# Optimization experiments

Measured on AMD Instinct MI355X. Metric: run time of the kernel, lower is better.

## Reference

```python
import jax, jax.numpy as jnp
import numpy as np

D_MODEL = 2048
N_HEADS = 32
N_KV_HEADS = 8
HEAD_DIM = D_MODEL // N_HEADS  # 64
N_REP = N_HEADS // N_KV_HEADS  # 4
SCALE = HEAD_DIM ** -0.5


def _rope_tables(seq_len):
    inv_freq = 1.0 / (10000.0 ** (jnp.arange(0, HEAD_DIM, 2, dtype=jnp.float32) / HEAD_DIM))
    t = jnp.arange(seq_len, dtype=jnp.float32)
    freqs = jnp.outer(t, inv_freq)  # [S, HEAD_DIM/2]
    return jnp.cos(freqs), jnp.sin(freqs)


def _apply_rope(x, cos, sin):
    # x: [b, h, s, d]; interleaved even/odd rotation, matching torch stack+flatten
    x_r, x_i = x[..., ::2], x[..., 1::2]
    out_r = x_r * cos - x_i * sin
    out_i = x_r * sin + x_i * cos
    out = jnp.stack([out_r, out_i], axis=-1)  # [b,h,s,d/2,2]
    return out.reshape(x.shape)


def setup_inputs() -> dict:
    key = jax.random.key(0)
    ks = jax.random.split(key, 5)
    bs, seq_len = 2, 2048
    std = D_MODEL ** -0.5
    x = jax.random.normal(ks[0], (bs, seq_len, D_MODEL), dtype=jnp.float32)
    wq = jax.random.normal(ks[1], (N_HEADS * HEAD_DIM, D_MODEL), dtype=jnp.float32) * std
    wk = jax.random.normal(ks[2], (N_KV_HEADS * HEAD_DIM, D_MODEL), dtype=jnp.float32) * std
    wv = jax.random.normal(ks[3], (N_KV_HEADS * HEAD_DIM, D_MODEL), dtype=jnp.float32) * std
    wo = jax.random.normal(ks[4], (D_MODEL, N_HEADS * HEAD_DIM), dtype=jnp.float32) * std
    return {"x": x, "wq": wq, "wk": wk, "wv": wv, "wo": wo}


def reference(x, wq, wk, wv, wo):
    bs, seq_len, _ = x.shape
    # fused-style QKV projections (nn.Linear: x @ W.T)
    q = (x @ wq.T).reshape(bs, seq_len, N_HEADS, HEAD_DIM).transpose(0, 2, 1, 3)
    k = (x @ wk.T).reshape(bs, seq_len, N_KV_HEADS, HEAD_DIM).transpose(0, 2, 1, 3)
    v = (x @ wv.T).reshape(bs, seq_len, N_KV_HEADS, HEAD_DIM).transpose(0, 2, 1, 3)
    cos, sin = _rope_tables(seq_len)  # [S, HEAD_DIM/2], broadcast over b,h
    q = _apply_rope(q, cos, sin)
    k = _apply_rope(k, cos, sin)
    # GQA: repeat KV heads to match Q heads
    k = jnp.repeat(k, N_REP, axis=1)  # [b, H, s, d]
    v = jnp.repeat(v, N_REP, axis=1)
    attn = jnp.einsum('bhqd,bhkd->bhqk', q, k) * SCALE
    causal = jnp.triu(jnp.ones((seq_len, seq_len), dtype=bool), k=1)
    attn = jnp.where(causal, -jnp.inf, attn)
    attn = jax.nn.softmax(attn, axis=-1)
    out = jnp.einsum('bhqk,bhkd->bhqd', attn, v)
    out = out.transpose(0, 2, 1, 3).reshape(bs, seq_len, D_MODEL)
    return out @ wo.T
```

## Files before the change

kernel.cpp:

```cpp
#include <hip/hip_runtime.h>

#define SEQ    2048
#define DM     2048
#define QKVN   3072
#define VTR    64

typedef short s16x8 __attribute__((ext_vector_type(8)));
typedef float f32x4 __attribute__((ext_vector_type(4)));
typedef unsigned short us;

#define MFMA(a,b,c) __builtin_amdgcn_mfma_f32_16x16x32_bf16((a),(b),(c),0,0,0)

__device__ __forceinline__ float bf2f(us u) {
    unsigned v = ((unsigned)u) << 16;
    return __builtin_bit_cast(float, v);
}
__device__ __forceinline__ us f2bf(float f) {
    unsigned u = __builtin_bit_cast(unsigned, f);
    u += 0x7FFFu + ((u >> 16) & 1u);
    return (us)(u >> 16);
}
__device__ __forceinline__ void stp(us* p, float f) {
    *p = (us)(__builtin_bit_cast(unsigned, f) >> 16);
}
__device__ __forceinline__ void glds16(const us* g, us* l) {
    __builtin_amdgcn_global_load_lds((__attribute__((address_space(1))) void*)g,
                                     (__attribute__((address_space(3))) void*)l, 16, 0, 0);
}

__global__ __launch_bounds__(256) void cvt_all(const float* __restrict__ x,
                                               const float* __restrict__ wq,
                                               const float* __restrict__ wk,
                                               const float* __restrict__ wv,
                                               const float* __restrict__ wo,
                                               us* __restrict__ xb,
                                               us* __restrict__ wdst) {
    int i = (blockIdx.x * blockDim.x + threadIdx.x) * 2;
    const float* src;
    int off;
    if (i < 2097152)      { src = x;  off = 0; }
    else {
        int j = i - 2097152;
        if (j < 1048576)      { src = wq; off = 2097152; }
        else if (j < 1310720) { src = wk; off = 2097152 + 1048576; }
        else if (j < 1572864) { src = wv; off = 2097152 + 1310720; }
        else                  { src = wo; off = 2097152 + 1572864; }
    }
    const int base = i - off;
    float4 v0 = ((const float4*)src)[base];
    float4 v1 = ((const float4*)src)[base + 1];
    s16x8 o;
    o[0] = (short)f2bf(v0.x); o[1] = (short)f2bf(v0.y);
    o[2] = (short)f2bf(v0.z); o[3] = (short)f2bf(v0.w);
    o[4] = (short)f2bf(v1.x); o[5] = (short)f2bf(v1.y);
    o[6] = (short)f2bf(v1.z); o[7] = (short)f2bf(v1.w);
    us* d = (i < 2097152) ? xb : wdst;
    const int di = (i < 2097152) ? i : i - 2097152;
    *(s16x8*)(d + di * 4) = o;
}

template <typename OutT, bool ROPE>
__global__ __launch_bounds__(512) void gemm_bt2(const us* __restrict__ A, const us* __restrict__ W,
                                                OutT* __restrict__ C, us* __restrict__ vt,
                                                int M, int N, int K) {
    __shared__ us lA[2][2][128 * 64];
    __shared__ us lB[2][2][128 * 64];
    const int tid = threadIdx.x, lane = tid & 63, wave = tid >> 6;
    const int quad = lane >> 4, lr = lane & 15;
    const int mh = wave >> 2;
    const int wnx = wave & 3;
    const int bh = wnx >> 1, br0 = (wnx & 1) * 64;
    const int m0 = blockIdx.x * 256, n0 = blockIdx.y * 256;

    const int srow = tid >> 3;
    const int scol = ((tid & 7) ^ (srow & 7)) * 8;
    const int sdst = srow * 64 + (tid & 7) * 8;

    const us* gA = A + (size_t)m0 * K;
    const us* gB = W + (size_t)n0 * K;

    auto stageH = [&](int s) {
        const int t = s >> 2, ty = s & 3, par = t & 1;
        const us* src;
        us* dst;
        if (ty < 2) { src = gA + (size_t)(ty * 128) * K;       dst = &lA[par][ty][0]; }
        else        { src = gB + (size_t)((ty - 2) * 128) * K; dst = &lB[par][ty - 2][0]; }
        src += t * 64;
        glds16(src + (size_t)srow * K + scol,        dst + sdst);
        glds16(src + (size_t)(srow + 64) * K + scol, dst + sdst + 64 * 64);
    };

    const int rsw = (lr & 7) << 3;
    auto rdA = [&](int par, int kk, int i) {
        return *(const s16x8*)&lA[par][mh][(i * 16 + lr) * 64 + ((kk * 32 + quad * 8) ^ rsw)];
    };
    auto rdB = [&](int par, int kk, int j) {
        return *(const s16x8*)&lB[par][bh][(br0 + j * 16 + lr) * 64 + ((kk * 32 + quad * 8) ^ rsw)];
    };

    f32x4 acc[8][4] = {};
    const int NT = K / 64;

    stageH(0); stageH(1); stageH(2); stageH(3); stageH(4);
    asm volatile("s_waitcnt vmcnt(2)" ::: "memory");
    __builtin_amdgcn_s_barrier();

    s16x8 af[2][4], ag[2][4], bfr[2][2], bg[2][2];
    for (int t = 0; t < NT; ++t) {
        const int par = t & 1;
#pragma unroll
        for (int kk = 0; kk < 2; kk++) {
#pragma unroll
            for (int i = 0; i < 4; i++) af[kk][i] = rdA(par, kk, i);
#pragma unroll
            for (int j = 0; j < 2; j++) bfr[kk][j] = rdB(par, kk, j);
        }
        if (t + 1 < NT) stageH(4 * (t + 1) + 1);
        __builtin_amdgcn_s_barrier();
        asm volatile("s_waitcnt lgkmcnt(0)" ::: "memory");
        __builtin_amdgcn_s_setprio(1);
#pragma unroll
        for (int i = 0; i < 4; i++)
#pragma unroll
            for (int j = 0; j < 2; j++)
#pragma unroll
                for (int kk = 0; kk < 2; kk++)
                    acc[i][j] = MFMA(af[kk][i], bfr[kk][j], acc[i][j]);
        __builtin_amdgcn_s_setprio(0);
        __builtin_amdgcn_s_barrier();
#pragma unroll
        for (int kk = 0; kk < 2; kk++)
#pragma unroll
            for (int j = 0; j < 2; j++) bg[kk][j] = rdB(par, kk, 2 + j);
        if (t + 1 < NT) stageH(4 * (t + 1) + 2);
        __builtin_amdgcn_s_barrier();
        asm volatile("s_waitcnt lgkmcnt(0)" ::: "memory");
        __builtin_amdgcn_s_setprio(1);
#pragma unroll
        for (int i = 0; i < 4; i++)
#pragma unroll
            for (int j = 0; j < 2; j++)
#pragma unroll
                for (int kk = 0; kk < 2; kk++)
                    acc[i][2 + j] = MFMA(af[kk][i], bg[kk][j], acc[i][2 + j]);
        __builtin_amdgcn_s_setprio(0);
        __builtin_amdgcn_s_barrier();
#pragma unroll
        for (int kk = 0; kk < 2; kk++)
#pragma unroll
            for (int i = 0; i < 4; i++) ag[kk][i] = rdA(par, kk, 4 + i);
        if (t + 1 < NT) stageH(4 * (t + 1) + 3);
        __builtin_amdgcn_s_barrier();
        asm volatile("s_waitcnt lgkmcnt(0)" ::: "memory");
        __builtin_amdgcn_s_setprio(1);
#pragma unroll
        for (int i = 0; i < 4; i++)
#pragma unroll
            for (int j = 0; j < 2; j++)
#pragma unroll
                for (int kk = 0; kk < 2; kk++)
                    acc[4 + i][j] = MFMA(ag[kk][i], bfr[kk][j], acc[4 + i][j]);
        __builtin_amdgcn_s_setprio(0);
        __builtin_amdgcn_s_barrier();
        if (t + 2 < NT) stageH(4 * (t + 2));
        __builtin_amdgcn_s_setprio(1);
#pragma unroll
        for (int i = 0; i < 4; i++)
#pragma unroll
            for (int j = 0; j < 2; j++)
#pragma unroll
                for (int kk = 0; kk < 2; kk++)
                    acc[4 + i][2 + j] = MFMA(ag[kk][i], bg[kk][j], acc[4 + i][2 + j]);
        __builtin_amdgcn_s_setprio(0);
        if (t + 1 < NT) {
            if (t + 2 < NT) asm volatile("s_waitcnt vmcnt(2)" ::: "memory");
            else            asm volatile("s_waitcnt vmcnt(0)" ::: "memory");
            __builtin_amdgcn_s_barrier();
        }
    }

    const bool vblk = ROPE && (n0 >= 2560);
#pragma unroll
    for (int i = 0; i < 8; i++)
#pragma unroll
        for (int j = 0; j < 4; j++) {
            const int row0 = m0 + mh * 128 + i * 16 + quad * 4;
            const int col  = n0 + wnx * 64 + j * 16 + lr;
            if (vblk) {
                const int d = col - 2560;
                const int b = row0 >> 11, s = row0 & (SEQ - 1);
                ushort4 o4;
                o4.x = f2bf(acc[i][j][0]); o4.y = f2bf(acc[i][j][1]);
                o4.z = f2bf(acc[i][j][2]); o4.w = f2bf(acc[i][j][3]);
                *(ushort4*)(vt + ((size_t)b * 512 + d) * SEQ + s) = o4;
            } else {
#pragma unroll
                for (int r = 0; r < 4; r++) {
                    const int row = row0 + r;
                    float v = acc[i][j][r];
                    if (ROPE && n0 < 2560) {
                        int pair = (col >> 1) & 31;
                        float inv = exp2f((float)pair * (-13.2877124f / 32.0f));
                        float ang = (float)(row & (SEQ - 1)) * inv;
                        float c = __cosf(ang), sn = __sinf(ang);
                        float p = __shfl_xor(v, 1);
                        v = v * c + ((col & 1) ? p * sn : -p * sn);
                    }
                    if constexpr (sizeof(OutT) == 2)
                        C[(size_t)row * N + col] = f2bf(v);
                    else
                        C[(size_t)row * N + col] = v;
                }
            }
        }
}

template <typename OutT>
__global__ __launch_bounds__(512) void gemm_bt2n(const us* __restrict__ A, const us* __restrict__ W,
                                                 OutT* __restrict__ C, int M, int N, int K) {
    __shared__ us lA[2][2][128 * 64];
    __shared__ us lB[2][128 * 64];
    const int tid = threadIdx.x, lane = tid & 63, wave = tid >> 6;
    const int quad = lane >> 4, lr = lane & 15;
    const int mh = wave >> 2;
    const int wnx = wave & 3;
    const int m0 = blockIdx.x * 256, n0 = blockIdx.y * 128;

    const int srow = tid >> 3;
    const int scol = ((tid & 7) ^ (srow & 7)) * 8;
    const int sdst = srow * 64 + (tid & 7) * 8;

    const us* gA = A + (size_t)m0 * K;
    const us* gB = W + (size_t)n0 * K;

    auto stageH = [&](int t, int ty) {
        const int par = t & 1;
        const us* src;
        us* dst;
        if (ty < 2) { src = gA + (size_t)(ty * 128) * K; dst = &lA[par][ty][0]; }
        else        { src = gB;                           dst = &lB[par][0]; }
        src += t * 64;
        glds16(src + (size_t)srow * K + scol,        dst + sdst);
        glds16(src + (size_t)(srow + 64) * K + scol, dst + sdst + 64 * 64);
    };

    const int rsw = (lr & 7) << 3;
    auto rdA = [&](int par, int kk, int i) {
        return *(const s16x8*)&lA[par][mh][(i * 16 + lr) * 64 + ((kk * 32 + quad * 8) ^ rsw)];
    };
    auto rdB = [&](int par, int kk, int j) {
        return *(const s16x8*)&lB[par][(wnx * 32 + j * 16 + lr) * 64 + ((kk * 32 + quad * 8) ^ rsw)];
    };

    f32x4 acc[8][2] = {};
    const int NT = K / 64;

    stageH(0, 0); stageH(0, 1); stageH(0, 2); stageH(1, 0);
    asm volatile("s_waitcnt vmcnt(2)" ::: "memory");
    __builtin_amdgcn_s_barrier();

    s16x8 af[2][4], ag[2][4], bfr[2][2];
    for (int t = 0; t < NT; ++t) {
        const int par = t & 1;
#pragma unroll
        for (int kk = 0; kk < 2; kk++) {
#pragma unroll
            for (int i = 0; i < 4; i++) af[kk][i] = rdA(par, kk, i);
#pragma unroll
            for (int j = 0; j < 2; j++) bfr[kk][j] = rdB(par, kk, j);
        }
        if (t + 1 < NT) stageH(t + 1, 1);
        __builtin_amdgcn_s_barrier();
        asm volatile("s_waitcnt lgkmcnt(0)" ::: "memory");
        __builtin_amdgcn_s_setprio(1);
#pragma unroll
        for (int i = 0; i < 4; i++)
#pragma unroll
            for (int j = 0; j < 2; j++)
#pragma unroll
                for (int kk = 0; kk < 2; kk++)
                    acc[i][j] = MFMA(af[kk][i], bfr[kk][j], acc[i][j]);
        __builtin_amdgcn_s_setprio(0);
        __builtin_amdgcn_s_barrier();
#pragma unroll
        for (int kk = 0; kk < 2; kk++)
#pragma unroll
            for (int i = 0; i < 4; i++) ag[kk][i] = rdA(par, kk, 4 + i);
        if (t + 1 < NT) stageH(t + 1, 2);
        __builtin_amdgcn_s_barrier();
        asm volatile("s_waitcnt lgkmcnt(0)" ::: "memory");
        __builtin_amdgcn_s_setprio(1);
#pragma unroll
        for (int i = 0; i < 4; i++)
#pragma unroll
            for (int j = 0; j < 2; j++)
#pragma unroll
                for (int kk = 0; kk < 2; kk++)
                    acc[4 + i][j] = MFMA(ag[kk][i], bfr[kk][j], acc[4 + i][j]);
        __builtin_amdgcn_s_setprio(0);
        if (t + 2 < NT) stageH(t + 2, 0);
        if (t + 1 < NT) {
            if (t + 2 < NT) asm volatile("s_waitcnt vmcnt(2)" ::: "memory");
            else            asm volatile("s_waitcnt vmcnt(0)" ::: "memory");
            __builtin_amdgcn_s_barrier();
        }
    }

#pragma unroll
    for (int i = 0; i < 8; i++)
#pragma unroll
        for (int j = 0; j < 2; j++)
#pragma unroll
            for (int r = 0; r < 4; r++) {
                int row = m0 + mh * 128 + i * 16 + quad * 4 + r;
                int col = n0 + wnx * 32 + j * 16 + lr;
                if constexpr (sizeof(OutT) == 2)
                    C[(size_t)row * N + col] = f2bf(acc[i][j][r]);
                else
                    C[(size_t)row * N + col] = acc[i][j][r];
            }
}

__global__ __launch_bounds__(256, 2) void flash_attn(const us* __restrict__ qkv,
                                                     const us* __restrict__ vt,
                                                     us* __restrict__ o) {
    __shared__ us P[4][4][16 * 72];
    const int bh = blockIdx.y, b = bh >> 5, h = bh & 31, kvh = h >> 2;
    const int wave = threadIdx.x >> 6, lane = threadIdx.x & 63;
    const int quad = lane >> 4, lr = lane & 15;
    const int p = ((int)blockIdx.x + (int)(blockIdx.y >> 3)) & 7;
    const int qts[4] = {p, 15 - p, 16 + p, 31 - p};
    const us* kbase = qkv + (size_t)b * SEQ * QKVN + 2048 + kvh * 64;
    const us* vb = vt + (size_t)(b * 8 + kvh) * VTR * SEQ;
    const float QS = 0.125f * 1.44269504f;

    s16x8 onesb;
    const short ov = (lr == 0) ? (short)0x3F80 : (short)0;
#pragma unroll
    for (int j = 0; j < 8; j++) onesb[j] = ov;

    int q0[4];
    s16x8 qa[4][2];
#pragma unroll
    for (int t = 0; t < 4; t++) {
        q0[t] = qts[t] * 64 + wave * 16;
        const us* qb = qkv + (size_t)(b * SEQ + q0[t]) * QKVN + h * 64;
        qa[t][0] = *(const s16x8*)(qb + (size_t)lr * QKVN + quad * 8);
        qa[t][1] = *(const s16x8*)(qb + (size_t)lr * QKVN + 32 + quad * 8);
#pragma unroll
        for (int j = 0; j < 8; j++) {
            qa[t][0][j] = (short)f2bf(bf2f((us)qa[t][0][j]) * QS);
            qa[t][1][j] = (short)f2bf(bf2f((us)qa[t][1][j]) * QS);
        }
    }

    f32x4 oacc[4][5] = {};
    s16x8 kf[8], vf[8];
    {
        const us* kp = kbase + (size_t)lr * QKVN;
#pragma unroll
        for (int nb = 0; nb < 4; nb++) {
            kf[2 * nb]     = *(const s16x8*)(kp + (size_t)nb * 16 * QKVN + quad * 8);
            kf[2 * nb + 1] = *(const s16x8*)(kp + (size_t)nb * 16 * QKVN + 32 + quad * 8);
        }
#pragma unroll
        for (int n = 0; n < 4; n++)
#pragma unroll
            for (int kc = 0; kc < 2; kc++)
                vf[n * 2 + kc] = *(const s16x8*)(vb + (size_t)(n * 16 + lr) * SEQ +
                                                 kc * 32 + quad * 8);
    }

    auto qk_tile = [&](int t, f32x4* sc) {
#pragma unroll
        for (int nb = 0; nb < 4; nb++) {
            sc[nb] = f32x4{0.f, 0.f, 0.f, 0.f};
            sc[nb] = MFMA(qa[t][0], kf[2 * nb], sc[nb]);
            sc[nb] = MFMA(qa[t][1], kf[2 * nb + 1], sc[nb]);
        }
    };
    auto store_tile = [&](int t, const f32x4* sc, int kb) {
        us* Pt = &P[wave][t][0];
        if (kb == qts[t]) {
#pragma unroll
            for (int nb = 0; nb < 4; nb++)
#pragma unroll
                for (int r = 0; r < 4; r++) {
                    int key = kb * 64 + nb * 16 + lr, row = q0[t] + quad * 4 + r;
                    float s = (key > row) ? -1e30f : sc[nb][r];
                    stp(&Pt[(quad * 4 + r) * 72 + nb * 16 + lr], exp2f(s));
                }
        } else {
#pragma unroll
            for (int nb = 0; nb < 4; nb++)
#pragma unroll
                for (int r = 0; r < 4; r++)
                    stp(&Pt[(quad * 4 + r) * 72 + nb * 16 + lr], exp2f(sc[nb][r]));
        }
    };

    const int kbmax = qts[3];
    for (int kb = 0; kb <= kbmax; kb++) {
        const bool a0 = (kb <= qts[0]), a1 = (kb <= qts[1]), a2 = (kb <= qts[2]);
        f32x4 sa[4], sb[4];
        if (a0) qk_tile(0, sa);
        if (a1) qk_tile(1, sb);
        if (a0) store_tile(0, sa, kb);
        if (a1) store_tile(1, sb, kb);
        if (a2) qk_tile(2, sa);
        qk_tile(3, sb);
        if (kb < kbmax) {
            const us* kp = kbase + (size_t)((kb + 1) * 64 + lr) * QKVN;
#pragma unroll
            for (int nb = 0; nb < 4; nb++) {
                kf[2 * nb]     = *(const s16x8*)(kp + (size_t)nb * 16 * QKVN + quad * 8);
                kf[2 * nb + 1] = *(const s16x8*)(kp + (size_t)nb * 16 * QKVN + 32 + quad * 8);
            }
        }
        if (a2) store_tile(2, sa, kb);
        store_tile(3, sb, kb);
        asm volatile("s_waitcnt lgkmcnt(0)" ::: "memory");
        __builtin_amdgcn_s_setprio(1);
#pragma unroll
        for (int t = 0; t < 4; t++) {
            if (kb <= qts[t]) {
#pragma unroll
                for (int kc = 0; kc < 2; kc++) {
                    s16x8 pa = *(const s16x8*)&P[wave][t][lr * 72 + kc * 32 + quad * 8];
#pragma unroll
                    for (int n = 0; n < 4; n++)
                        oacc[t][n] = MFMA(pa, vf[n * 2 + kc], oacc[t][n]);
                    oacc[t][4] = MFMA(pa, onesb, oacc[t][4]);
                }
            }
        }
        __builtin_amdgcn_s_setprio(0);
        if (kb < kbmax) {
#pragma unroll
            for (int n = 0; n < 4; n++)
#pragma unroll
                for (int kc = 0; kc < 2; kc++)
                    vf[n * 2 + kc] = *(const s16x8*)(vb + (size_t)(n * 16 + lr) * SEQ +
                                                     (kb + 1) * 64 + kc * 32 + quad * 8);
        }
    }

#pragma unroll
    for (int t = 0; t < 4; t++)
#pragma unroll
        for (int r = 0; r < 4; r++) {
            float l = __shfl(oacc[t][4][r], lane & 48);
            float li = 1.0f / l;
#pragma unroll
            for (int n = 0; n < 4; n++)
                o[(size_t)(b * SEQ + q0[t] + quad * 4 + r) * DM + h * 64 + n * 16 + lr] =
                    f2bf(oacc[t][n][r] * li);
        }
}

extern "C" void kernel_launch(void* const* d_in, const int* in_sizes, int n_in,
                              void* d_out, int out_size, void* d_ws, size_t ws_size,
                              hipStream_t stream) {
    const float* x  = (const float*)d_in[0];
    const float* wq = (const float*)d_in[1];
    const float* wk = (const float*)d_in[2];
    const float* wv = (const float*)d_in[3];
    const float* wo = (const float*)d_in[4];
    float* out = (float*)d_out;

    char* ws = (char*)d_ws;
    const size_t MB = 1024 * 1024;
    us* xb     = (us*)(ws + 0 * MB);
    us* abuf   = (us*)(ws + 0 * MB);
    us* wqkvb  = (us*)(ws + 16 * MB);
    us* wob    = (us*)(ws + 28 * MB);
    us* qkvbuf = (us*)(ws + 36 * MB);
    us* vtbuf  = (us*)(ws + 60 * MB);

    dim3 blk(256);
    cvt_all<<<dim3(9216), blk, 0, stream>>>(x, wq, wk, wv, wo, xb, wqkvb);

    gemm_bt2<us, true><<<dim3(16, 12), dim3(512), 0, stream>>>(xb, wqkvb, qkvbuf, vtbuf,
                                                               4096, 3072, 2048);
    flash_attn<<<dim3(8, 64), blk, 0, stream>>>(qkvbuf, vtbuf, abuf);
    gemm_bt2n<float><<<dim3(16, 16), dim3(512), 0, stream>>>(abuf, wob, out, 4096, 2048, 2048);
}
```

Baseline: 339.8 us.

## Rewrite flash attention with 32x32 MFMA and register-resident P via lane shuffles

Rewrites the attention kernel to use 32x32x16 bf16 MFMA tiles. Scores are computed as K·Q so that the exponentiated probabilities stay in registers and are repacked into A-operand layout with packed bf16 converts and cross-half lane shuffles, instead of a round trip through shared memory. Row sums are accumulated in VALU rather than with an extra MFMA against a ones vector. Each wave now handles two balanced 32-row query tiles instead of four 16-row tiles. The change removes LDS traffic and the waitcnt stall, but adds shuffle and VALU work and halves the per-wave query reuse of each K/V load.

```diff
diff --git a/kernel.cpp b/kernel.cpp
--- a/kernel.cpp
+++ b/kernel.cpp
@@ -7,9 +7,12 @@
 
 typedef short s16x8 __attribute__((ext_vector_type(8)));
 typedef float f32x4 __attribute__((ext_vector_type(4)));
+typedef float f32x16 __attribute__((ext_vector_type(16)));
+typedef unsigned u32x4 __attribute__((ext_vector_type(4)));
 typedef unsigned short us;
 
-#define MFMA(a,b,c) __builtin_amdgcn_mfma_f32_16x16x32_bf16((a),(b),(c),0,0,0)
+#define MFMA(a,b,c)   __builtin_amdgcn_mfma_f32_16x16x32_bf16((a),(b),(c),0,0,0)
+#define MFMA32(a,b,c) __builtin_amdgcn_mfma_f32_32x32x16_bf16((a),(b),(c),0,0,0)
 
 __device__ __forceinline__ float bf2f(us u) {
     unsigned v = ((unsigned)u) << 16;
@@ -20,8 +23,10 @@
     u += 0x7FFFu + ((u >> 16) & 1u);
     return (us)(u >> 16);
 }
-__device__ __forceinline__ void stp(us* p, float f) {
-    *p = (us)(__builtin_bit_cast(unsigned, f) >> 16);
+__device__ __forceinline__ unsigned cvtpk(float lo, float hi) {
+    unsigned r;
+    asm("v_cvt_pk_bf16_f32 %0, %1, %2" : "=v"(r) : "v"(lo), "v"(hi));
+    return r;
 }
 __device__ __forceinline__ void glds16(const us* g, us* l) {
     __builtin_amdgcn_global_load_lds((__attribute__((address_space(1))) void*)g,
@@ -324,138 +329,115 @@
 __global__ __launch_bounds__(256, 2) void flash_attn(const us* __restrict__ qkv,
                                                      const us* __restrict__ vt,
                                                      us* __restrict__ o) {
-    __shared__ us P[4][4][16 * 72];
     const int bh = blockIdx.y, b = bh >> 5, h = bh & 31, kvh = h >> 2;
     const int wave = threadIdx.x >> 6, lane = threadIdx.x & 63;
-    const int quad = lane >> 4, lr = lane & 15;
-    const int p = ((int)blockIdx.x + (int)(blockIdx.y >> 3)) & 7;
-    const int qts[4] = {p, 15 - p, 16 + p, 31 - p};
+    const int half = lane >> 5, l5 = lane & 31;
+    const int jb = ((int)blockIdx.x + (int)(blockIdx.y >> 3)) & 7;
+    const int j = jb * 4 + wave;
+    const int q00 = j * 32, q01 = (63 - j) * 32;
+    const int kbm0 = j, kbm1 = 63 - j;
     const us* kbase = qkv + (size_t)b * SEQ * QKVN + 2048 + kvh * 64;
     const us* vb = vt + (size_t)(b * 8 + kvh) * VTR * SEQ;
     const float QS = 0.125f * 1.44269504f;
 
-    s16x8 onesb;
-    const short ov = (lr == 0) ? (short)0x3F80 : (short)0;
-#pragma unroll
-    for (int j = 0; j < 8; j++) onesb[j] = ov;
-
-    int q0[4];
-    s16x8 qa[4][2];
-#pragma unroll
-    for (int t = 0; t < 4; t++) {
-        q0[t] = qts[t] * 64 + wave * 16;
-        const us* qb = qkv + (size_t)(b * SEQ + q0[t]) * QKVN + h * 64;
-        qa[t][0] = *(const s16x8*)(qb + (size_t)lr * QKVN + quad * 8);
-        qa[t][1] = *(const s16x8*)(qb + (size_t)lr * QKVN + 32 + quad * 8);
-#pragma unroll
-        for (int j = 0; j < 8; j++) {
-            qa[t][0][j] = (short)f2bf(bf2f((us)qa[t][0][j]) * QS);
-            qa[t][1][j] = (short)f2bf(bf2f((us)qa[t][1][j]) * QS);
-        }
-    }
-
-    f32x4 oacc[4][5] = {};
-    s16x8 kf[8], vf[8];
-    {
-        const us* kp = kbase + (size_t)lr * QKVN;
-#pragma unroll
-        for (int nb = 0; nb < 4; nb++) {
-            kf[2 * nb]     = *(const s16x8*)(kp + (size_t)nb * 16 * QKVN + quad * 8);
-            kf[2 * nb + 1] = *(const s16x8*)(kp + (size_t)nb * 16 * QKVN + 32 + quad * 8);
-        }
-#pragma unroll
-        for (int n = 0; n < 4; n++)
-#pragma unroll
-            for (int kc = 0; kc < 2; kc++)
-                vf[n * 2 + kc] = *(const s16x8*)(vb + (size_t)(n * 16 + lr) * SEQ +
-                                                 kc * 32 + quad * 8);
-    }
-
-    auto qk_tile = [&](int t, f32x4* sc) {
-#pragma unroll
-        for (int nb = 0; nb < 4; nb++) {
-            sc[nb] = f32x4{0.f, 0.f, 0.f, 0.f};
-            sc[nb] = MFMA(qa[t][0], kf[2 * nb], sc[nb]);
-            sc[nb] = MFMA(qa[t][1], kf[2 * nb + 1], sc[nb]);
-        }
-    };
-    auto store_tile = [&](int t, const f32x4* sc, int kb) {
-        us* Pt = &P[wave][t][0];
-        if (kb == qts[t]) {
-#pragma unroll
-            for (int nb = 0; nb < 4; nb++)
-#pragma unroll
-                for (int r = 0; r < 4; r++) {
-                    int key = kb * 64 + nb * 16 + lr, row = q0[t] + quad * 4 + r;
-                    float s = (key > row) ? -1e30f : sc[nb][r];
-                    stp(&Pt[(quad * 4 + r) * 72 + nb * 16 + lr], exp2f(s));
-                }
+    s16x8 qf[2][4];
+#pragma unroll
+    for (int t = 0; t < 2; t++) {
+        const int q0t = t ? q01 : q00;
+        const us* qb = qkv + (size_t)(b * SEQ + q0t + l5) * QKVN + h * 64 + half * 8;
+#pragma unroll
+        for (int dc = 0; dc < 4; dc++) {
+            qf[t][dc] = *(const s16x8*)(qb + dc * 16);
+#pragma unroll
+            for (int e = 0; e < 8; e++)
+                qf[t][dc][e] = (short)f2bf(bf2f((us)qf[t][dc][e]) * QS);
+        }
+    }
+
+    f32x16 oacc[2][2] = {};
+    float lsum0 = 0.f, lsum1 = 0.f;
+
+    s16x8 kf[4], vf[4];
+    auto load_k = [&](int kb) {
+        const us* kp = kbase + (size_t)(kb * 32 + l5) * QKVN + half * 8;
+#pragma unroll
+        for (int dc = 0; dc < 4; dc++) kf[dc] = *(const s16x8*)(kp + dc * 16);
+    };
+    auto load_v = [&](int kb) {
+#pragma unroll
+        for (int kc = 0; kc < 2; kc++)
+#pragma unroll
+            for (int dh = 0; dh < 2; dh++)
+                vf[kc * 2 + dh] = *(const s16x8*)(vb + (size_t)(dh * 32 + l5) * SEQ +
+                                                  kb * 32 + kc * 16 + half * 8);
+    };
+    load_k(0);
+    load_v(0);
+
+    auto tilepv = [&](int kb, int kbt, int q0t, f32x16& sc, float& ls,
+                      f32x16& od0, f32x16& od1) {
+        float p[16];
+        if (kb == kbt) {
+#pragma unroll
+            for (int r = 0; r < 16; r++) {
+                int key = kb * 32 + (r & 3) + 8 * (r >> 2) + 4 * half;
+                float s = (key > q0t + l5) ? -1e30f : sc[r];
+                p[r] = exp2f(s);
+                ls += p[r];
+            }
         } else {
 #pragma unroll
-            for (int nb = 0; nb < 4; nb++)
-#pragma unroll
-                for (int r = 0; r < 4; r++)
-                    stp(&Pt[(quad * 4 + r) * 72 + nb * 16 + lr], exp2f(sc[nb][r]));
-        }
-    };
-
-    const int kbmax = qts[3];
-    for (int kb = 0; kb <= kbmax; kb++) {
-        const bool a0 = (kb <= qts[0]), a1 = (kb <= qts[1]), a2 = (kb <= qts[2]);
-        f32x4 sa[4], sb[4];
-        if (a0) qk_tile(0, sa);
-        if (a1) qk_tile(1, sb);
-        if (a0) store_tile(0, sa, kb);
-        if (a1) store_tile(1, sb, kb);
-        if (a2) qk_tile(2, sa);
-        qk_tile(3, sb);
-        if (kb < kbmax) {
-            const us* kp = kbase + (size_t)((kb + 1) * 64 + lr) * QKVN;
-#pragma unroll
-            for (int nb = 0; nb < 4; nb++) {
-                kf[2 * nb]     = *(const s16x8*)(kp + (size_t)nb * 16 * QKVN + quad * 8);
-                kf[2 * nb + 1] = *(const s16x8*)(kp + (size_t)nb * 16 * QKVN + 32 + quad * 8);
+            for (int r = 0; r < 16; r++) { p[r] = exp2f(sc[r]); ls += p[r]; }
+        }
+        unsigned pr[8], sw[8];
+#pragma unroll
+        for (int i = 0; i < 8; i++) pr[i] = cvtpk(p[2 * i], p[2 * i + 1]);
+#pragma unroll
+        for (int i = 0; i < 8; i++) sw[i] = __shfl_xor(pr[i], 32);
+        u32x4 w0, w1;
+        w0[0] = half ? sw[2] : pr[0]; w0[1] = half ? sw[3] : pr[1];
+        w0[2] = half ? pr[2] : sw[0]; w0[3] = half ? pr[3] : sw[1];
+        w1[0] = half ? sw[6] : pr[4]; w1[1] = half ? sw[7] : pr[5];
+        w1[2] = half ? pr[6] : sw[4]; w1[3] = half ? pr[7] : sw[5];
+        s16x8 fa0 = __builtin_bit_cast(s16x8, w0);
+        s16x8 fa1 = __builtin_bit_cast(s16x8, w1);
+        od0 = MFMA32(fa0, vf[0], od0);
+        od0 = MFMA32(fa1, vf[2], od0);
+        od1 = MFMA32(fa0, vf[1], od1);
+        od1 = MFMA32(fa1, vf[3], od1);
+    };
+
+    for (int kb = 0; kb <= kbm1; kb++) {
+        const bool a0 = (kb <= kbm0);
+        f32x16 s0 = {}, s1 = {};
+        if (a0) {
+#pragma unroll
+            for (int dc = 0; dc < 4; dc++) s0 = MFMA32(kf[dc], qf[0][dc], s0);
+        }
+#pragma unroll
+        for (int dc = 0; dc < 4; dc++) s1 = MFMA32(kf[dc], qf[1][dc], s1);
+        if (kb < kbm1) load_k(kb + 1);
+        if (a0) tilepv(kb, kbm0, q00, s0, lsum0, oacc[0][0], oacc[0][1]);
+        tilepv(kb, kbm1, q01, s1, lsum1, oacc[1][0], oacc[1][1]);
+        if (kb < kbm1) load_v(kb + 1);
+    }
+
+#pragma unroll
+    for (int t = 0; t < 2; t++) {
+        const float lsel = t ? lsum1 : lsum0;
+        const int q0t = t ? q01 : q00;
+        const float lf = lsel + __shfl_xor(lsel, 32);
+#pragma unroll
+        for (int r = 0; r < 16; r++) {
+            const int qrow = (r & 3) + 8 * (r >> 2) + 4 * half;
+            const float li = 1.0f / __shfl(lf, qrow);
+#pragma unroll
+            for (int dh = 0; dh < 2; dh++) {
+                const float v = (t ? oacc[1][dh][r] : oacc[0][dh][r]) * li;
+                o[(size_t)(b * SEQ + q0t + qrow) * DM + h * 64 + dh * 32 + l5] = f2bf(v);
             }
         }
-        if (a2) store_tile(2, sa, kb);
-        store_tile(3, sb, kb);
-        asm volatile("s_waitcnt lgkmcnt(0)" ::: "memory");
-        __builtin_amdgcn_s_setprio(1);
-#pragma unroll
-        for (int t = 0; t < 4; t++) {
-            if (kb <= qts[t]) {
-#pragma unroll
-                for (int kc = 0; kc < 2; kc++) {
-                    s16x8 pa = *(const s16x8*)&P[wave][t][lr * 72 + kc * 32 + quad * 8];
-#pragma unroll
-                    for (int n = 0; n < 4; n++)
-                        oacc[t][n] = MFMA(pa, vf[n * 2 + kc], oacc[t][n]);
-                    oacc[t][4] = MFMA(pa, onesb, oacc[t][4]);
-                }
-            }
-        }
-        __builtin_amdgcn_s_setprio(0);
-        if (kb < kbmax) {
-#pragma unroll
-            for (int n = 0; n < 4; n++)
-#pragma unroll
-                for (int kc = 0; kc < 2; kc++)
-                    vf[n * 2 + kc] = *(const s16x8*)(vb + (size_t)(n * 16 + lr) * SEQ +
-                                                     (kb + 1) * 64 + kc * 32 + quad * 8);
-        }
-    }
-
-#pragma unroll
-    for (int t = 0; t < 4; t++)
-#pragma unroll
-        for (int r = 0; r < 4; r++) {
-            float l = __shfl(oacc[t][4][r], lane & 48);
-            float li = 1.0f / l;
-#pragma unroll
-            for (int n = 0; n < 4; n++)
-                o[(size_t)(b * SEQ + q0[t] + quad * 4 + r) * DM + h * 64 + n * 16 + lr] =
-                    f2bf(oacc[t][n][r] * li);
-        }
+    }
 }
 
 extern "C" void kernel_launch(void* const* d_in, const int* in_sizes, int n_in,
```

After: 329.2 us. 3.1% less time.
